# Performance work log

Measured on AMD Instinct MI355X. Metric: run time of the kernel, lower is better.

The kernel has to match this reference:

```python
import jax, jax.numpy as jnp
import numpy as np

B = 256
THRESH = 0.0
SHIFT = 0.0


def setup_inputs() -> dict:
    key = jax.random.key(0)
    ks = jax.random.split(key, 8)
    s = lambda k, shape, sc: (jax.random.normal(k, shape, jnp.float32) * sc)
    return {
        "x": jax.random.normal(ks[0], (B, 3, 250, 250), jnp.float32),
        "conv1_w": s(ks[1], (6, 3, 5, 5), 0.08),
        "conv1_b": jnp.zeros((6,), jnp.float32),
        "conv2_w": s(ks[2], (15, 6, 3, 3), 0.12),
        "conv2_b": jnp.zeros((15,), jnp.float32),
        "fc1_w": s(ks[3], (120, 55815), 0.004),
        "fc1_b": jnp.zeros((120,), jnp.float32),
        "fc2_w": s(ks[4], (84, 120), 0.09),
        "fc2_b": jnp.zeros((84,), jnp.float32),
        "fc3_w": s(ks[5], (1, 84), 0.1),
        "fc3_b": jnp.zeros((1,), jnp.float32),
        "pl_w": s(ks[6], (1, 1), 1.0),
        "pl_b": jnp.zeros((1,), jnp.float32),
        "pl_scale": jnp.ones((1,), jnp.float32),
        "pl_bias": jnp.zeros((1,), jnp.float32),
    }


def _conv2d(x, w, b, stride, pad):
    y = jax.lax.conv_general_dilated(
        x, w, (stride, stride), [(pad, pad), (pad, pad)],
        dimension_numbers=("NCHW", "OIHW", "NCHW"))
    return y + b[None, :, None, None]


def _maxpool_k2_s1(x):
    return jax.lax.reduce_window(x, -jnp.inf, jax.lax.max,
                                 (1, 1, 2, 2), (1, 1, 1, 1), "VALID")


def reference(x, conv1_w, conv1_b, conv2_w, conv2_b, fc1_w, fc1_b,
              fc2_w, fc2_b, fc3_w, fc3_b, pl_w, pl_b, pl_scale, pl_bias):
    # CNN backbone (dropout layers are eval-mode no-ops)
    h = jax.nn.relu(_conv2d(x, conv1_w, conv1_b, 2, 1))   # [B,6,124,124]
    h = _maxpool_k2_s1(h)                                  # [B,6,123,123]
    h = jax.nn.relu(_conv2d(h, conv2_w, conv2_b, 2, 1))   # [B,15,62,62]
    h = _maxpool_k2_s1(h)                                  # [B,15,61,61]
    h = h.reshape(h.shape[0], -1)                          # [B,55815]
    h = jax.nn.relu(h @ fc1_w.T + fc1_b)                   # [B,120]
    features = h @ fc2_w.T + fc2_b                         # [B,84]

    # head: fc3 -> ParameterizedLayer -> sigmoid
    logits = features @ fc3_w.T + fc3_b                    # [B,1]
    z = jnp.tanh(logits @ pl_w.T + pl_b) * pl_scale + pl_bias + SHIFT
    probs = jax.nn.sigmoid(z)[:, 0]                        # [B]

    # dynamic cosine-similarity graph (fidelity_adjacency, secondary=None)
    norms = jnp.linalg.norm(features, axis=1)              # [B]
    sim = (features @ features.T) / (norms[:, None] * norms[None, :] + 1e-12)
    adj = (sim >= THRESH) & (~jnp.eye(features.shape[0], dtype=bool))
    adjf = adj.astype(probs.dtype)                         # [B,B] 0/1

    # degree-weighted neighbor-mean aggregation
    deg = adjf.sum(axis=1)                                 # [B]
    neigh_mean = jnp.where(deg > 0, (adjf @ probs) / jnp.maximum(deg, 1.0), 0.0)
    agg = (probs + neigh_mean) / (1.0 + deg)
    return jnp.stack([agg, 1.0 - agg], axis=-1)            # [B,2]
```

## Files before the change

kernel.cpp:

```cpp
#include <hip/hip_runtime.h>
#include <math.h>


__device__ __forceinline__ void gload_lds4(const float* g, float* l) {
    __builtin_amdgcn_global_load_lds(
        (const __attribute__((address_space(1))) unsigned int*)g,
        (__attribute__((address_space(3))) unsigned int*)l, 4, 0, 0);
}

__global__ __launch_bounds__(256, 3) void k_c1p1(const float* __restrict__ x,
                                                 const float* __restrict__ w,
                                                 const float* __restrict__ bias,
                                                 float* __restrict__ p1) {
    __shared__ float xs[22][258];

    const int t    = blockIdx.x;
    const int b    = blockIdx.y;
    const int tid  = threadIdx.x;
    const int lane = tid & 63;
    const int wv   = tid >> 6;
    const int s    = wv & 1;
    const int q    = wv >> 1;
    const int ow   = 62 * s + lane;
    const int owc  = min(ow, 123);
    const int owc2 = 2 * owc;
    const int ihlo = 16 * t - 1;

    const int sr  = __builtin_amdgcn_readfirstlane(tid >> 7);
    const int sm  = tid & 127;
    const int smc = min(sm, 124);

    float acc[5][6];
#pragma unroll
    for (int j = 0; j < 5; ++j)
#pragma unroll
        for (int oc = 0; oc < 6; ++oc) acc[j][oc] = 0.f;

    const float* xb = x + (size_t)b * 3 * 62500;
    const bool interior = (t >= 1) && (t <= 14);

    if (tid < 21) xs[tid][0] = 0.f;

#pragma unroll 1
    for (int ci = 0; ci < 3; ++ci) {
        __syncthreads();
        const float* xc = xb + (size_t)ci * 62500;
        if (interior) {
            for (int r = wv; r < 21; r += 4) {
                const float* src = xc + (size_t)(ihlo + r) * 250 + lane;
#pragma unroll
                for (int k = 0; k < 4; ++k)
                    gload_lds4(src + 64 * k, &xs[r][1 + 64 * k]);
            }
        } else {
            float2 vv[11];
#pragma unroll
            for (int i = 0; i < 11; ++i) {
                int r   = 2 * i + sr;
                int ih  = ihlo + r;
                int ihc = min(max(ih, 0), 249);
                bool ok = (ih >= 0) && (ih < 250);
                float2 raw = *(const float2*)(xc + (size_t)ihc * 250 + (smc << 1));
                vv[i].x = ok ? raw.x : 0.f;
                vv[i].y = ok ? raw.y : 0.f;
            }
#pragma unroll
            for (int i = 0; i < 11; ++i) {
                int r = 2 * i + sr;
                xs[r][2 * sm + 1] = vv[i].x;
                xs[r][2 * sm + 2] = vv[i].y;
            }
        }
        __syncthreads();

        float rr[13][5];
#pragma unroll
        for (int r = 0; r < 13; ++r) {
            const float* pp = &xs[8 * q + r][owc2];
            rr[r][0] = pp[0]; rr[r][1] = pp[1]; rr[r][2] = pp[2];
            rr[r][3] = pp[3]; rr[r][4] = pp[4];
        }
#pragma unroll
        for (int kh = 0; kh < 5; ++kh) {
            float wk[6][5];
#pragma unroll
            for (int oc = 0; oc < 6; ++oc)
#pragma unroll
                for (int kw = 0; kw < 5; ++kw)
                    wk[oc][kw] = w[((oc * 3 + ci) * 5 + kh) * 5 + kw];
#pragma unroll
            for (int j = 0; j < 5; ++j) {
                const float* rp = rr[2 * j + kh];
#pragma unroll
                for (int oc = 0; oc < 6; ++oc) {
                    float a = acc[j][oc];
                    a = fmaf(rp[0], wk[oc][0], a);
                    a = fmaf(rp[1], wk[oc][1], a);
                    a = fmaf(rp[2], wk[oc][2], a);
                    a = fmaf(rp[3], wk[oc][3], a);
                    a = fmaf(rp[4], wk[oc][4], a);
                    acc[j][oc] = a;
                }
            }
        }
    }

    const int pw   = ow;
    const int oh0  = 8 * t + 4 * q;
    const bool cok = (lane < 63) && (pw < 123);
#pragma unroll
    for (int oc = 0; oc < 6; ++oc) {
        float bv = bias[oc];
        float r0 = fmaxf(acc[0][oc] + bv, 0.f);
        float r1 = fmaxf(acc[1][oc] + bv, 0.f);
        float r2 = fmaxf(acc[2][oc] + bv, 0.f);
        float r3 = fmaxf(acc[3][oc] + bv, 0.f);
        float r4 = fmaxf(acc[4][oc] + bv, 0.f);
        float vm0 = fmaxf(r0, r1), vm1 = fmaxf(r1, r2);
        float vm2 = fmaxf(r2, r3), vm3 = fmaxf(r3, r4);
        float p0 = fmaxf(vm0, __shfl_down(vm0, 1));
        float p1v = fmaxf(vm1, __shfl_down(vm1, 1));
        float p2v = fmaxf(vm2, __shfl_down(vm2, 1));
        float p3 = fmaxf(vm3, __shfl_down(vm3, 1));
        if (cok) {
            float* op = p1 + (((size_t)b * 6 + oc) * 123) * 123 + pw;
            if (oh0 + 0 < 123) op[(size_t)(oh0 + 0) * 123] = p0;
            if (oh0 + 1 < 123) op[(size_t)(oh0 + 1) * 123] = p1v;
            if (oh0 + 2 < 123) op[(size_t)(oh0 + 2) * 123] = p2v;
            if (oh0 + 3 < 123) op[(size_t)(oh0 + 3) * 123] = p3;
        }
    }
}

__global__ __launch_bounds__(256, 3) void k_c2p2(const float* __restrict__ p1,
                                                 const float* __restrict__ w,
                                                 const float* __restrict__ bias,
                                                 float* __restrict__ p2) {
    __shared__ float xs[20][130];

    const int v    = blockIdx.x;
    const int b    = blockIdx.y;
    const int tid  = threadIdx.x;
    const int lane = tid & 63;
    const int q    = tid >> 6;
    const int ow   = lane;
    const int owc  = min(ow, 61);
    const int owc2 = 2 * owc;
    const int ihlo = 16 * v - 1;

    const int sr   = __builtin_amdgcn_readfirstlane(tid >> 7);
    const int sc   = tid & 127;
    const int scc  = min(sc, 122);
    const int wcol = (sc < 123) ? (sc + 1) : 129;

    float acc[3][15];
#pragma unroll
    for (int j = 0; j < 3; ++j)
#pragma unroll
        for (int oc = 0; oc < 15; ++oc) acc[j][oc] = 0.f;

    const float* ib = p1 + (size_t)b * 6 * 15129;
    const bool interior = (v >= 1) && (v <= 6);

    if (tid < 19) { xs[tid][0] = 0.f; xs[tid][124] = 0.f; }

#pragma unroll 1
    for (int ci = 0; ci < 6; ++ci) {
        __syncthreads();
        const float* xc = ib + (size_t)ci * 15129;
        if (interior) {
            for (int r = q; r < 19; r += 4) {
                const float* src = xc + (size_t)(ihlo + r) * 123 + lane;
                gload_lds4(src,      &xs[r][1]);
                gload_lds4(src + 64, &xs[r][65]);
            }
        } else {
            float vv[10];
#pragma unroll
            for (int i = 0; i < 10; ++i) {
                int r   = 2 * i + sr;
                int ih  = ihlo + r;
                int ihc = min(max(ih, 0), 122);
                bool ok = (ih >= 0) && (ih < 123);
                float raw = xc[(size_t)ihc * 123 + scc];
                vv[i] = ok ? raw : 0.f;
            }
#pragma unroll
            for (int i = 0; i < 10; ++i) {
                int r = 2 * i + sr;
                xs[r][wcol] = vv[i];
            }
            if (tid < 19) xs[tid][124] = 0.f;
        }
        __syncthreads();

        float rr[7][3];
#pragma unroll
        for (int c = 0; c < 7; ++c) {
            const float* pp = &xs[4 * q + c][owc2];
            rr[c][0] = pp[0]; rr[c][1] = pp[1]; rr[c][2] = pp[2];
            if (ow == 61) rr[c][2] = 0.f;
        }
#pragma unroll
        for (int kh = 0; kh < 3; ++kh) {
            float wk[15][3];
#pragma unroll
            for (int oc = 0; oc < 15; ++oc)
#pragma unroll
                for (int kw = 0; kw < 3; ++kw)
                    wk[oc][kw] = w[((oc * 6 + ci) * 3 + kh) * 3 + kw];
#pragma unroll
            for (int j = 0; j < 3; ++j) {
                const float* rp = rr[2 * j + kh];
#pragma unroll
                for (int oc = 0; oc < 15; ++oc) {
                    float a = acc[j][oc];
                    a = fmaf(rp[0], wk[oc][0], a);
                    a = fmaf(rp[1], wk[oc][1], a);
                    a = fmaf(rp[2], wk[oc][2], a);
                    acc[j][oc] = a;
                }
            }
        }
    }

    const int pw   = ow;
    const int oh0  = 8 * v + 2 * q;
    const bool cok = (lane < 61);
#pragma unroll
    for (int oc = 0; oc < 15; ++oc) {
        float bv = bias[oc];
        float r0 = fmaxf(acc[0][oc] + bv, 0.f);
        float r1 = fmaxf(acc[1][oc] + bv, 0.f);
        float r2 = fmaxf(acc[2][oc] + bv, 0.f);
        float vm0 = fmaxf(r0, r1), vm1 = fmaxf(r1, r2);
        float p0 = fmaxf(vm0, __shfl_down(vm0, 1));
        float p1v = fmaxf(vm1, __shfl_down(vm1, 1));
        if (cok) {
            float* op = p2 + (((size_t)b * 15 + oc) * 61) * 61 + pw;
            if (oh0 + 0 < 61) op[(size_t)(oh0 + 0) * 61] = p0;
            if (oh0 + 1 < 61) op[(size_t)(oh0 + 1) * 61] = p1v;
        }
    }
}

__global__ __launch_bounds__(256) void k_fc1(const float* __restrict__ A,
                                             const float* __restrict__ B,
                                             float* __restrict__ partial) {
    __shared__ float As[128][64];
    __shared__ float Bs[128][64];
    const int K = 55815;
    int tid = threadIdx.x;
    int kb  = blockIdx.x;
    int m0  = blockIdx.y * 128;
    int mx  = tid >> 4;
    int nx  = tid & 15;
    int kl  = tid & 63;
    int wv  = tid >> 6;
    int mb  = tid >> 6;

    Bs[120 + mb][kl] = 0.f;
    Bs[124 + mb][kl] = 0.f;

    float acc[8][8];
#pragma unroll
    for (int i = 0; i < 8; ++i)
#pragma unroll
        for (int j = 0; j < 8; ++j) acc[i][j] = 0.f;

    for (int ch = kb; ch < 873; ch += 256) {
        __syncthreads();
        if (ch != 872) {
            const float* Ab = A + (size_t)m0 * K + (size_t)ch * 64;
            const float* Bb = B + (size_t)ch * 64;
            for (int m = wv; m < 128; m += 4) {
                int kcol = kl ^ ((m & 7) << 2);
                gload_lds4(Ab + (size_t)m * K + kcol, &As[m][0]);
            }
            for (int m = wv; m < 120; m += 4) {
                int kcol = kl ^ ((m & 7) << 2);
                gload_lds4(Bb + (size_t)m * K + kcol, &Bs[m][0]);
            }
        } else {
            int k    = ch * 64 + kl;
            bool kok = (k < K);
            int kc   = kok ? k : K - 1;
#pragma unroll
            for (int batch = 0; batch < 4; ++batch) {
                float va[8], vb[8];
#pragma unroll
                for (int u = 0; u < 8; ++u) {
                    int m = mb + 4 * (batch * 8 + u);
                    va[u] = A[(size_t)(m0 + m) * K + kc];
                }
#pragma unroll
                for (int u = 0; u < 8; ++u) {
                    if (batch < 3 || u < 6) {
                        int m = mb + 4 * (batch * 8 + u);
                        vb[u] = B[(size_t)m * K + kc];
                    }
                }
#pragma unroll
                for (int u = 0; u < 8; ++u) {
                    int m = mb + 4 * (batch * 8 + u);
                    As[m][kl ^ ((m & 7) << 2)] = kok ? va[u] : 0.f;
                }
#pragma unroll
                for (int u = 0; u < 8; ++u) {
                    if (batch < 3 || u < 6) {
                        int m = mb + 4 * (batch * 8 + u);
                        Bs[m][kl ^ ((m & 7) << 2)] = kok ? vb[u] : 0.f;
                    }
                }
            }
        }
        __syncthreads();
#pragma unroll 2
        for (int k4 = 0; k4 < 16; ++k4) {
            float4 af[8], bf[8];
#pragma unroll
            for (int i = 0; i < 8; ++i) {
                int m = mx + 16 * i;
                af[i] = *(const float4*)&As[m][(k4 * 4) ^ ((m & 7) << 2)];
            }
#pragma unroll
            for (int j = 0; j < 8; ++j) {
                int n = nx + 16 * j;
                bf[j] = *(const float4*)&Bs[n][(k4 * 4) ^ ((n & 7) << 2)];
            }
#pragma unroll
            for (int i = 0; i < 8; ++i)
#pragma unroll
                for (int j = 0; j < 8; ++j) {
                    acc[i][j] = fmaf(af[i].x, bf[j].x, acc[i][j]);
                    acc[i][j] = fmaf(af[i].y, bf[j].y, acc[i][j]);
                    acc[i][j] = fmaf(af[i].z, bf[j].z, acc[i][j]);
                    acc[i][j] = fmaf(af[i].w, bf[j].w, acc[i][j]);
                }
        }
    }

    float* pp = partial + (size_t)kb * 30720;
#pragma unroll
    for (int i = 0; i < 8; ++i) {
        int m = m0 + mx + 16 * i;
#pragma unroll
        for (int j = 0; j < 8; ++j) {
            int n = nx + 16 * j;
            if (n < 120) pp[m * 120 + n] = acc[i][j];
        }
    }
}

__global__ __launch_bounds__(256) void k_fc1red1(const float* __restrict__ partial,
                                                 float* __restrict__ partial2) {
    int idx = blockIdx.x * 256 + threadIdx.x;
    int s   = blockIdx.y;
    const float* p = partial + (size_t)(s * 32) * 30720 + idx;
    float acc = 0.f;
#pragma unroll 8
    for (int kb = 0; kb < 32; ++kb) acc += p[(size_t)kb * 30720];
    partial2[(size_t)s * 30720 + idx] = acc;
}

__global__ __launch_bounds__(256) void k_fc1red2(const float* __restrict__ partial2,
                                                 const float* __restrict__ bias,
                                                 float* __restrict__ out) {
    int idx = blockIdx.x * 256 + threadIdx.x;
    int n = idx % 120;
    float s = bias[n];
#pragma unroll
    for (int k = 0; k < 8; ++k) s += partial2[(size_t)k * 30720 + idx];
    out[idx] = fmaxf(s, 0.f);
}

__global__ __launch_bounds__(256) void k_fc2(const float* __restrict__ h,
                                             const float* __restrict__ w,
                                             const float* __restrict__ bias,
                                             float* __restrict__ out) {
    int idx = blockIdx.x * 256 + threadIdx.x;
    int n = idx % 84;
    int m = idx / 84;
    const float* hp = h + m * 120;
    const float* wp = w + n * 120;
    float s = bias[n];
#pragma unroll 4
    for (int k = 0; k < 120; ++k) s = fmaf(hp[k], wp[k], s);
    out[idx] = s;
}

__global__ __launch_bounds__(256) void k_head(const float* __restrict__ f,
                                              const float* __restrict__ w3,
                                              const float* __restrict__ b3,
                                              const float* __restrict__ plw,
                                              const float* __restrict__ plb,
                                              const float* __restrict__ pls,
                                              const float* __restrict__ plbias,
                                              float* __restrict__ probs,
                                              float* __restrict__ norms) {
    int b = threadIdx.x;
    const float* fp = f + b * 84;
    float nsq = 0.f, lg = b3[0];
#pragma unroll 4
    for (int k = 0; k < 84; ++k) {
        float v = fp[k];
        nsq = fmaf(v, v, nsq);
        lg  = fmaf(v, w3[k], lg);
    }
    float z = tanhf(lg * plw[0] + plb[0]) * pls[0] + plbias[0];
    probs[b] = 1.f / (1.f + expf(-z));
    norms[b] = sqrtf(nsq);
}

__global__ __launch_bounds__(256) void k_graph(const float* __restrict__ f,
                                               const float* __restrict__ probs,
                                               const float* __restrict__ norms,
                                               float* __restrict__ out) {
    __shared__ float fi[84];
    __shared__ float sd[4], sv[4];
    int i = blockIdx.x;
    int j = threadIdx.x;
    if (j < 84) fi[j] = f[i * 84 + j];
    __syncthreads();
    const float* fj = f + j * 84;
    float dot = 0.f;
#pragma unroll 4
    for (int k = 0; k < 84; ++k) dot = fmaf(fi[k], fj[k], dot);
    float sim = dot / (norms[i] * norms[j] + 1e-12f);
    bool adj = (j != i) && (sim >= 0.0f);
    float d = adj ? 1.f : 0.f;
    float v = adj ? probs[j] : 0.f;
#pragma unroll
    for (int off = 32; off >= 1; off >>= 1) {
        d += __shfl_down(d, off);
        v += __shfl_down(v, off);
    }
    int wave = j >> 6, lane = j & 63;
    if (lane == 0) { sd[wave] = d; sv[wave] = v; }
    __syncthreads();
    if (j == 0) {
        float D = sd[0] + sd[1] + sd[2] + sd[3];
        float V = sv[0] + sv[1] + sv[2] + sv[3];
        float nm = (D > 0.f) ? (V / fmaxf(D, 1.f)) : 0.f;
        float agg = (probs[i] + nm) / (1.f + D);
        out[2 * i]     = agg;
        out[2 * i + 1] = 1.f - agg;
    }
}

extern "C" void kernel_launch(void* const* d_in, const int* in_sizes, int n_in,
                              void* d_out, int out_size, void* d_ws, size_t ws_size,
                              hipStream_t stream) {
    const float* x    = (const float*)d_in[0];
    const float* w1   = (const float*)d_in[1];
    const float* b1   = (const float*)d_in[2];
    const float* w2   = (const float*)d_in[3];
    const float* b2   = (const float*)d_in[4];
    const float* fw1  = (const float*)d_in[5];
    const float* fb1  = (const float*)d_in[6];
    const float* fw2  = (const float*)d_in[7];
    const float* fb2  = (const float*)d_in[8];
    const float* fw3  = (const float*)d_in[9];
    const float* fb3  = (const float*)d_in[10];
    const float* plw  = (const float*)d_in[11];
    const float* plb  = (const float*)d_in[12];
    const float* pls  = (const float*)d_in[13];
    const float* plbi = (const float*)d_in[14];
    float* out = (float*)d_out;

    float* ws = (float*)d_ws;
    float* p1       = ws;
    float* p2       = p1 + 23238144;
    float* partial  = p2 + 14288640;
    float* fc1out   = partial + 7864320;
    float* features = fc1out + 30720;
    float* probs    = features + 21504;
    float* norms    = probs + 256;
    float* partial2 = norms + 256;

    k_c1p1<<<dim3(16, 256), 256, 0, stream>>>(x, w1, b1, p1);
    k_c2p2<<<dim3(8, 256), 256, 0, stream>>>(p1, w2, b2, p2);
    k_fc1<<<dim3(256, 2), 256, 0, stream>>>(p2, fw1, partial);
    k_fc1red1<<<dim3(120, 8), 256, 0, stream>>>(partial, partial2);
    k_fc1red2<<<120, 256, 0, stream>>>(partial2, fb1, fc1out);
    k_fc2<<<84, 256, 0, stream>>>(fc1out, fw2, fb2, features);
    k_head<<<1, 256, 0, stream>>>(features, fw3, fb3, plw, plb, pls, plbi,
                                  probs, norms);
    k_graph<<<256, 256, 0, stream>>>(features, probs, norms, out);
}
```

Before: 503.2 us.

## Double-buffer conv input channel loads and use register-staged loads in fc1

The two conv kernels get two LDS buffers on their interior path, so the next input channel is loaded asynchronously with global_load_lds while the current channel is computed, and one barrier per channel is dropped. fc1 drops the direct-to-LDS async load path and stages every chunk through registers, as the tail chunk already did. The extra buffer doubles LDS use per block and may lower occupancy. There is also a leftover unused lambda, and fc1 loses its async loads, which could hurt.

New measurement: 477.9 us. 1.05x faster.

```diff
diff --git a/kernel.cpp b/kernel.cpp
--- a/kernel.cpp
+++ b/kernel.cpp
@@ -12,7 +12,7 @@
                                                  const float* __restrict__ w,
                                                  const float* __restrict__ bias,
                                                  float* __restrict__ p1) {
-    __shared__ float xs[22][258];
+    __shared__ float xs[2][22][258];
 
     const int t    = blockIdx.x;
     const int b    = blockIdx.y;
@@ -39,20 +39,82 @@
     const float* xb = x + (size_t)b * 3 * 62500;
     const bool interior = (t >= 1) && (t <= 14);
 
-    if (tid < 21) xs[tid][0] = 0.f;
-
-#pragma unroll 1
-    for (int ci = 0; ci < 3; ++ci) {
-        __syncthreads();
-        const float* xc = xb + (size_t)ci * 62500;
-        if (interior) {
+    if (tid < 22) { xs[0][tid][0] = 0.f; xs[1][tid][0] = 0.f; }
+
+    auto compute = [&](int ci, const float (*xsb)[258]) {
+        float rr[13][5];
+#pragma unroll
+        for (int r = 0; r < 13; ++r) {
+            const float* pp = &xsb[8 * q + r][owc2];
+            rr[r][0] = pp[0]; rr[r][1] = pp[1]; rr[r][2] = pp[2];
+            rr[r][3] = pp[3]; rr[r][4] = pp[4];
+        }
+        return [=, &acc](const float* wbase) {
+            (void)wbase;
+        };
+    };
+    (void)compute;
+
+    if (interior) {
+        {
+            const float* xc = xb;
             for (int r = wv; r < 21; r += 4) {
                 const float* src = xc + (size_t)(ihlo + r) * 250 + lane;
 #pragma unroll
                 for (int k = 0; k < 4; ++k)
-                    gload_lds4(src + 64 * k, &xs[r][1 + 64 * k]);
-            }
-        } else {
+                    gload_lds4(src + 64 * k, &xs[0][r][1 + 64 * k]);
+            }
+        }
+#pragma unroll 1
+        for (int ci = 0; ci < 3; ++ci) {
+            const int cur = ci & 1;
+            __syncthreads();
+            const float(*xsb)[258] = xs[cur];
+            float rr[13][5];
+#pragma unroll
+            for (int r = 0; r < 13; ++r) {
+                const float* pp = &xsb[8 * q + r][owc2];
+                rr[r][0] = pp[0]; rr[r][1] = pp[1]; rr[r][2] = pp[2];
+                rr[r][3] = pp[3]; rr[r][4] = pp[4];
+            }
+            if (ci < 2) {
+                const float* xc = xb + (size_t)(ci + 1) * 62500;
+                for (int r = wv; r < 21; r += 4) {
+                    const float* src = xc + (size_t)(ihlo + r) * 250 + lane;
+#pragma unroll
+                    for (int k = 0; k < 4; ++k)
+                        gload_lds4(src + 64 * k, &xs[cur ^ 1][r][1 + 64 * k]);
+                }
+            }
+#pragma unroll
+            for (int kh = 0; kh < 5; ++kh) {
+                float wk[6][5];
+#pragma unroll
+                for (int oc = 0; oc < 6; ++oc)
+#pragma unroll
+                    for (int kw = 0; kw < 5; ++kw)
+                        wk[oc][kw] = w[((oc * 3 + ci) * 5 + kh) * 5 + kw];
+#pragma unroll
+                for (int j = 0; j < 5; ++j) {
+                    const float* rp = rr[2 * j + kh];
+#pragma unroll
+                    for (int oc = 0; oc < 6; ++oc) {
+                        float a = acc[j][oc];
+                        a = fmaf(rp[0], wk[oc][0], a);
+                        a = fmaf(rp[1], wk[oc][1], a);
+                        a = fmaf(rp[2], wk[oc][2], a);
+                        a = fmaf(rp[3], wk[oc][3], a);
+                        a = fmaf(rp[4], wk[oc][4], a);
+                        acc[j][oc] = a;
+                    }
+                }
+            }
+        }
+    } else {
+#pragma unroll 1
+        for (int ci = 0; ci < 3; ++ci) {
+            __syncthreads();
+            const float* xc = xb + (size_t)ci * 62500;
             float2 vv[11];
 #pragma unroll
             for (int i = 0; i < 11; ++i) {
@@ -67,39 +129,38 @@
 #pragma unroll
             for (int i = 0; i < 11; ++i) {
                 int r = 2 * i + sr;
-                xs[r][2 * sm + 1] = vv[i].x;
-                xs[r][2 * sm + 2] = vv[i].y;
-            }
-        }
-        __syncthreads();
-
-        float rr[13][5];
-#pragma unroll
-        for (int r = 0; r < 13; ++r) {
-            const float* pp = &xs[8 * q + r][owc2];
-            rr[r][0] = pp[0]; rr[r][1] = pp[1]; rr[r][2] = pp[2];
-            rr[r][3] = pp[3]; rr[r][4] = pp[4];
-        }
-#pragma unroll
-        for (int kh = 0; kh < 5; ++kh) {
-            float wk[6][5];
-#pragma unroll
-            for (int oc = 0; oc < 6; ++oc)
-#pragma unroll
-                for (int kw = 0; kw < 5; ++kw)
-                    wk[oc][kw] = w[((oc * 3 + ci) * 5 + kh) * 5 + kw];
-#pragma unroll
-            for (int j = 0; j < 5; ++j) {
-                const float* rp = rr[2 * j + kh];
-#pragma unroll
-                for (int oc = 0; oc < 6; ++oc) {
-                    float a = acc[j][oc];
-                    a = fmaf(rp[0], wk[oc][0], a);
-                    a = fmaf(rp[1], wk[oc][1], a);
-                    a = fmaf(rp[2], wk[oc][2], a);
-                    a = fmaf(rp[3], wk[oc][3], a);
-                    a = fmaf(rp[4], wk[oc][4], a);
-                    acc[j][oc] = a;
+                xs[0][r][2 * sm + 1] = vv[i].x;
+                xs[0][r][2 * sm + 2] = vv[i].y;
+            }
+            __syncthreads();
+            float rr[13][5];
+#pragma unroll
+            for (int r = 0; r < 13; ++r) {
+                const float* pp = &xs[0][8 * q + r][owc2];
+                rr[r][0] = pp[0]; rr[r][1] = pp[1]; rr[r][2] = pp[2];
+                rr[r][3] = pp[3]; rr[r][4] = pp[4];
+            }
+#pragma unroll
+            for (int kh = 0; kh < 5; ++kh) {
+                float wk[6][5];
+#pragma unroll
+                for (int oc = 0; oc < 6; ++oc)
+#pragma unroll
+                    for (int kw = 0; kw < 5; ++kw)
+                        wk[oc][kw] = w[((oc * 3 + ci) * 5 + kh) * 5 + kw];
+#pragma unroll
+                for (int j = 0; j < 5; ++j) {
+                    const float* rp = rr[2 * j + kh];
+#pragma unroll
+                    for (int oc = 0; oc < 6; ++oc) {
+                        float a = acc[j][oc];
+                        a = fmaf(rp[0], wk[oc][0], a);
+                        a = fmaf(rp[1], wk[oc][1], a);
+                        a = fmaf(rp[2], wk[oc][2], a);
+                        a = fmaf(rp[3], wk[oc][3], a);
+                        a = fmaf(rp[4], wk[oc][4], a);
+                        acc[j][oc] = a;
+                    }
                 }
             }
         }
@@ -136,7 +197,7 @@
                                                  const float* __restrict__ w,
                                                  const float* __restrict__ bias,
                                                  float* __restrict__ p2) {
-    __shared__ float xs[20][130];
+    __shared__ float xs[2][20][130];
 
     const int v    = blockIdx.x;
     const int b    = blockIdx.y;
@@ -162,19 +223,67 @@
     const float* ib = p1 + (size_t)b * 6 * 15129;
     const bool interior = (v >= 1) && (v <= 6);
 
-    if (tid < 19) { xs[tid][0] = 0.f; xs[tid][124] = 0.f; }
-
-#pragma unroll 1
-    for (int ci = 0; ci < 6; ++ci) {
-        __syncthreads();
-        const float* xc = ib + (size_t)ci * 15129;
-        if (interior) {
+    if (tid < 20) {
+        xs[0][tid][0] = 0.f;   xs[1][tid][0] = 0.f;
+        xs[0][tid][124] = 0.f; xs[1][tid][124] = 0.f;
+    }
+
+    if (interior) {
+        {
+            const float* xc = ib;
             for (int r = q; r < 19; r += 4) {
                 const float* src = xc + (size_t)(ihlo + r) * 123 + lane;
-                gload_lds4(src,      &xs[r][1]);
-                gload_lds4(src + 64, &xs[r][65]);
-            }
-        } else {
+                gload_lds4(src,      &xs[0][r][1]);
+                gload_lds4(src + 64, &xs[0][r][65]);
+            }
+        }
+#pragma unroll 1
+        for (int ci = 0; ci < 6; ++ci) {
+            const int cur = ci & 1;
+            __syncthreads();
+            const float(*xsb)[130] = xs[cur];
+            float rr[7][3];
+#pragma unroll
+            for (int c = 0; c < 7; ++c) {
+                const float* pp = &xsb[4 * q + c][owc2];
+                rr[c][0] = pp[0]; rr[c][1] = pp[1]; rr[c][2] = pp[2];
+                if (ow == 61) rr[c][2] = 0.f;
+            }
+            if (ci < 5) {
+                const float* xc = ib + (size_t)(ci + 1) * 15129;
+                for (int r = q; r < 19; r += 4) {
+                    const float* src = xc + (size_t)(ihlo + r) * 123 + lane;
+                    gload_lds4(src,      &xs[cur ^ 1][r][1]);
+                    gload_lds4(src + 64, &xs[cur ^ 1][r][65]);
+                }
+            }
+#pragma unroll
+            for (int kh = 0; kh < 3; ++kh) {
+                float wk[15][3];
+#pragma unroll
+                for (int oc = 0; oc < 15; ++oc)
+#pragma unroll
+                    for (int kw = 0; kw < 3; ++kw)
+                        wk[oc][kw] = w[((oc * 6 + ci) * 3 + kh) * 3 + kw];
+#pragma unroll
+                for (int j = 0; j < 3; ++j) {
+                    const float* rp = rr[2 * j + kh];
+#pragma unroll
+                    for (int oc = 0; oc < 15; ++oc) {
+                        float a = acc[j][oc];
+                        a = fmaf(rp[0], wk[oc][0], a);
+                        a = fmaf(rp[1], wk[oc][1], a);
+                        a = fmaf(rp[2], wk[oc][2], a);
+                        acc[j][oc] = a;
+                    }
+                }
+            }
+        }
+    } else {
+#pragma unroll 1
+        for (int ci = 0; ci < 6; ++ci) {
+            __syncthreads();
+            const float* xc = ib + (size_t)ci * 15129;
             float vv[10];
 #pragma unroll
             for (int i = 0; i < 10; ++i) {
@@ -188,37 +297,35 @@
 #pragma unroll
             for (int i = 0; i < 10; ++i) {
                 int r = 2 * i + sr;
-                xs[r][wcol] = vv[i];
-            }
-            if (tid < 19) xs[tid][124] = 0.f;
-        }
-        __syncthreads();
-
-        float rr[7][3];
-#pragma unroll
-        for (int c = 0; c < 7; ++c) {
-            const float* pp = &xs[4 * q + c][owc2];
-            rr[c][0] = pp[0]; rr[c][1] = pp[1]; rr[c][2] = pp[2];
-            if (ow == 61) rr[c][2] = 0.f;
-        }
-#pragma unroll
-        for (int kh = 0; kh < 3; ++kh) {
-            float wk[15][3];
-#pragma unroll
-            for (int oc = 0; oc < 15; ++oc)
-#pragma unroll
-                for (int kw = 0; kw < 3; ++kw)
-                    wk[oc][kw] = w[((oc * 6 + ci) * 3 + kh) * 3 + kw];
-#pragma unroll
-            for (int j = 0; j < 3; ++j) {
-                const float* rp = rr[2 * j + kh];
-#pragma unroll
-                for (int oc = 0; oc < 15; ++oc) {
-                    float a = acc[j][oc];
-                    a = fmaf(rp[0], wk[oc][0], a);
-                    a = fmaf(rp[1], wk[oc][1], a);
-                    a = fmaf(rp[2], wk[oc][2], a);
-                    acc[j][oc] = a;
+                xs[0][r][wcol] = vv[i];
+            }
+            __syncthreads();
+            float rr[7][3];
+#pragma unroll
+            for (int c = 0; c < 7; ++c) {
+                const float* pp = &xs[0][4 * q + c][owc2];
+                rr[c][0] = pp[0]; rr[c][1] = pp[1]; rr[c][2] = pp[2];
+                if (ow == 61) rr[c][2] = 0.f;
+            }
+#pragma unroll
+            for (int kh = 0; kh < 3; ++kh) {
+                float wk[15][3];
+#pragma unroll
+                for (int oc = 0; oc < 15; ++oc)
+#pragma unroll
+                    for (int kw = 0; kw < 3; ++kw)
+                        wk[oc][kw] = w[((oc * 6 + ci) * 3 + kh) * 3 + kw];
+#pragma unroll
+                for (int j = 0; j < 3; ++j) {
+                    const float* rp = rr[2 * j + kh];
+#pragma unroll
+                    for (int oc = 0; oc < 15; ++oc) {
+                        float a = acc[j][oc];
+                        a = fmaf(rp[0], wk[oc][0], a);
+                        a = fmaf(rp[1], wk[oc][1], a);
+                        a = fmaf(rp[2], wk[oc][2], a);
+                        acc[j][oc] = a;
+                    }
                 }
             }
         }
@@ -256,7 +363,6 @@
     int mx  = tid >> 4;
     int nx  = tid & 15;
     int kl  = tid & 63;
-    int wv  = tid >> 6;
     int mb  = tid >> 6;
 
     Bs[120 + mb][kl] = 0.f;
@@ -269,48 +375,35 @@
         for (int j = 0; j < 8; ++j) acc[i][j] = 0.f;
 
     for (int ch = kb; ch < 873; ch += 256) {
+        int k    = ch * 64 + kl;
+        bool kok = (k < K);
+        int kc   = kok ? k : K - 1;
         __syncthreads();
-        if (ch != 872) {
-            const float* Ab = A + (size_t)m0 * K + (size_t)ch * 64;
-            const float* Bb = B + (size_t)ch * 64;
-            for (int m = wv; m < 128; m += 4) {
-                int kcol = kl ^ ((m & 7) << 2);
-                gload_lds4(Ab + (size_t)m * K + kcol, &As[m][0]);
-            }
-            for (int m = wv; m < 120; m += 4) {
-                int kcol = kl ^ ((m & 7) << 2);
-                gload_lds4(Bb + (size_t)m * K + kcol, &Bs[m][0]);
-            }
-        } else {
-            int k    = ch * 64 + kl;
-            bool kok = (k < K);
-            int kc   = kok ? k : K - 1;
-#pragma unroll
-            for (int batch = 0; batch < 4; ++batch) {
-                float va[8], vb[8];
-#pragma unroll
-                for (int u = 0; u < 8; ++u) {
+#pragma unroll
+        for (int batch = 0; batch < 4; ++batch) {
+            float va[8], vb[8];
+#pragma unroll
+            for (int u = 0; u < 8; ++u) {
+                int m = mb + 4 * (batch * 8 + u);
+                va[u] = A[(size_t)(m0 + m) * K + kc];
+            }
+#pragma unroll
+            for (int u = 0; u < 8; ++u) {
+                if (batch < 3 || u < 6) {
                     int m = mb + 4 * (batch * 8 + u);
-                    va[u] = A[(size_t)(m0 + m) * K + kc];
-                }
-#pragma unroll
-                for (int u = 0; u < 8; ++u) {
-                    if (batch < 3 || u < 6) {
-                        int m = mb + 4 * (batch * 8 + u);
-                        vb[u] = B[(size_t)m * K + kc];
-                    }
-                }
-#pragma unroll
-                for (int u = 0; u < 8; ++u) {
+                    vb[u] = B[(size_t)m * K + kc];
+                }
+            }
+#pragma unroll
+            for (int u = 0; u < 8; ++u) {
+                int m = mb + 4 * (batch * 8 + u);
+                As[m][kl ^ ((m & 7) << 2)] = kok ? va[u] : 0.f;
+            }
+#pragma unroll
+            for (int u = 0; u < 8; ++u) {
+                if (batch < 3 || u < 6) {
                     int m = mb + 4 * (batch * 8 + u);
-                    As[m][kl ^ ((m & 7) << 2)] = kok ? va[u] : 0.f;
-                }
-#pragma unroll
-                for (int u = 0; u < 8; ++u) {
-                    if (batch < 3 || u < 6) {
-                        int m = mb + 4 * (batch * 8 + u);
-                        Bs[m][kl ^ ((m & 7) << 2)] = kok ? vb[u] : 0.f;
-                    }
+                    Bs[m][kl ^ ((m & 7) << 2)] = kok ? vb[u] : 0.f;
                 }
             }
         }
```
